# Optimization experiments

Measured on AMD Instinct MI355X. Metric: run time of the kernel, lower is better.

Reference implementation:

```python
import jax, jax.numpy as jnp
import numpy as np

B, S, DIM = 4, 2048, 1024


def _xavier(key, shape):
    # xavier_uniform for a [out, in] Linear weight
    fan_in, fan_out = shape[1], shape[0]
    limit = float(np.sqrt(6.0 / (fan_in + fan_out)))
    return jax.random.uniform(key, shape, jnp.float32, -limit, limit)


def setup_inputs() -> dict:
    key = jax.random.key(0)
    ks = jax.random.split(key, 8)
    z_real = jax.random.normal(ks[0], (B, S, DIM), jnp.float32)
    z_imag = jax.random.normal(ks[1], (B, S, DIM), jnp.float32)
    wq_r = _xavier(ks[2], (DIM, DIM))
    wq_i = _xavier(ks[3], (DIM, DIM))
    wk_r = _xavier(ks[4], (DIM, DIM))
    wk_i = _xavier(ks[5], (DIM, DIM))
    wv_r = _xavier(ks[6], (DIM, DIM))
    wv_i = _xavier(ks[7], (DIM, DIM))
    # causal mask (0 = masked), broadcast over batch
    mask = jnp.tril(jnp.ones((S, S), jnp.int32))
    return {"z_real": z_real, "z_imag": z_imag,
            "wq_r": wq_r, "wq_i": wq_i,
            "wk_r": wk_r, "wk_i": wk_i,
            "wv_r": wv_r, "wv_i": wv_i,
            "mask": mask}


def _complex_linear(xr, xi, wr, wi):
    # torch Linear: y = x @ W^T
    yr = xr @ wr.T - xi @ wi.T
    yi = xi @ wr.T + xr @ wi.T
    return yr, yi


def reference(z_real, z_imag, wq_r, wq_i, wk_r, wk_i, wv_r, wv_i, mask):
    dim = z_real.shape[-1]
    scale = dim ** (-0.5)
    qr, qi = _complex_linear(z_real, z_imag, wq_r, wq_i)
    kr, ki = _complex_linear(z_real, z_imag, wk_r, wk_i)
    vr, vi = _complex_linear(z_real, z_imag, wv_r, wv_i)
    # cat([q.real, q.imag]) @ cat([k.real, k.imag])^T == qr@kr^T + qi@ki^T
    scores = (jnp.einsum('bsd,btd->bst', qr, kr)
              + jnp.einsum('bsd,btd->bst', qi, ki)) * scale  # [B,S,S]
    scores = jnp.where(mask == 0, -jnp.inf, scores)
    attn = jax.nn.softmax(scores, axis=-1)
    out_r = jnp.einsum('bst,btd->bsd', attn, vr)
    out_i = jnp.einsum('bst,btd->bsd', attn, vi)
    return jnp.stack([out_r, out_i], axis=0)  # [2,B,S,dim] = (real, imag)
```

## Files before the change

kernel.cpp:

```cpp
#include <hip/hip_runtime.h>
#include <hip/hip_bf16.h>
#include <hip/hip_fp16.h>

#define DIMK 1024
#define SEQ  2048
#define BATCH 4
#define NTOK (BATCH*SEQ)
#define PROJ_ELEMS ((size_t)NTOK*DIMK)
#define LD 2048

typedef unsigned short ushort_t;
typedef __attribute__((ext_vector_type(8))) short short8;
typedef __attribute__((ext_vector_type(4))) float float4v;

__device__ __forceinline__ unsigned short f2bf(float f) {
    union { float f; unsigned int i; } x; x.f = f;
    unsigned int r = x.i + 0x7fffu + ((x.i >> 16) & 1u);
    return (unsigned short)(r >> 16);
}

__device__ __forceinline__ void gld_lds16(const void* g, void* l) {
    auto gp = reinterpret_cast<const __attribute__((address_space(1))) unsigned int*>(
        reinterpret_cast<uintptr_t>(g));
    auto lp = reinterpret_cast<__attribute__((address_space(3))) unsigned int*>(
        reinterpret_cast<uintptr_t>(l));
    __builtin_amdgcn_global_load_lds(gp, lp, 16, 0, 0);
}

__device__ __forceinline__ void gemm_core(
    const ushort_t* __restrict__ Arow,
    const ushort_t* __restrict__ Brow,
    int kbeg, int kend,
    ushort_t* Asm, ushort_t* Bsm,
    float4v acc[4][4], int wave, int lane)
{
    const int g  = lane >> 2;
    const int sx = lane & 3;
    const int scol = (((sx - (g >> 1)) & 3)) * 8;
    const int sc0 = wave * 2, sc1 = wave * 2 + 1;
    const int r16  = lane & 15;
    const int quad = lane >> 4;
    const int swz  = ((quad + (r16 >> 1)) & 3) * 8;
    const int cA = (wave >> 1) * 4;
    const int cB = (wave & 1) * 4;

    for (int k0 = kbeg; k0 < kend; k0 += 64) {
        #pragma unroll
        for (int h = 0; h < 2; ++h) {
            const int kh = k0 + h * 32;
            ushort_t* Ah = Asm + h * 4096;
            ushort_t* Bh = Bsm + h * 4096;
            gld_lds16(Arow + (size_t)(sc0 * 16 + g) * LD + kh + scol, Ah + sc0 * 512);
            gld_lds16(Arow + (size_t)(sc1 * 16 + g) * LD + kh + scol, Ah + sc1 * 512);
            gld_lds16(Brow + (size_t)(sc0 * 16 + g) * LD + kh + scol, Bh + sc0 * 512);
            gld_lds16(Brow + (size_t)(sc1 * 16 + g) * LD + kh + scol, Bh + sc1 * 512);
        }
        __syncthreads();
        #pragma unroll
        for (int h = 0; h < 2; ++h) {
            const ushort_t* Ah = Asm + h * 4096;
            const ushort_t* Bh = Bsm + h * 4096;
            short8 af[4], bfr[4];
            #pragma unroll
            for (int i = 0; i < 4; ++i)
                af[i] = *(const short8*)(Ah + (cA + i) * 512 + r16 * 32 + swz);
            #pragma unroll
            for (int j = 0; j < 4; ++j)
                bfr[j] = *(const short8*)(Bh + (cB + j) * 512 + r16 * 32 + swz);
            #pragma unroll
            for (int i = 0; i < 4; ++i)
                #pragma unroll
                for (int j = 0; j < 4; ++j)
                    acc[i][j] = __builtin_amdgcn_mfma_f32_16x16x32_bf16(af[i], bfr[j], acc[i][j], 0, 0, 0);
        }
        __syncthreads();
    }
}

__global__ __launch_bounds__(256, 2)
void gemm_proj(const ushort_t* __restrict__ A, const ushort_t* __restrict__ B,
               ushort_t* __restrict__ Cq, ushort_t* __restrict__ Ck,
               ushort_t* __restrict__ Cv)
{
    __shared__ ushort_t Asm[128 * 64], Bsm[128 * 64];
    const int tid = threadIdx.x, wave = tid >> 6, lane = tid & 63;
    const int m0 = blockIdx.y * 128;
    const int n0g = blockIdx.x * 128;
    ushort_t* C = (n0g < 2048) ? Cq : ((n0g < 4096) ? Ck : Cv);
    const int n0 = n0g & 2047;
    float4v acc[4][4] = {};
    gemm_core(A + (size_t)m0 * LD, B + (size_t)n0g * LD, 0, 2048, Asm, Bsm, acc, wave, lane);

    const int wm = (wave >> 1) * 64, wn = (wave & 1) * 64;
    const int col16 = lane & 15, quad = lane >> 4;
    #pragma unroll
    for (int i = 0; i < 4; ++i)
        #pragma unroll
        for (int j = 0; j < 4; ++j) {
            const int n = n0 + wn + j * 16 + col16;
            #pragma unroll
            for (int r = 0; r < 4; ++r) {
                const int m = m0 + wm + i * 16 + quad * 4 + r;
                C[(size_t)m * LD + n] = f2bf(acc[i][j][r]);
            }
        }
}

__global__ __launch_bounds__(256, 2)
void gemm_scores(const ushort_t* __restrict__ Q, const ushort_t* __restrict__ K,
                 __half* __restrict__ S)
{
    const int jt = blockIdx.x, it = blockIdx.y, b = blockIdx.z;
    if (jt > it) return;
    __shared__ ushort_t Asm[128 * 64], Bsm[128 * 64];
    const int tid = threadIdx.x, wave = tid >> 6, lane = tid & 63;
    const size_t boff = (size_t)b * SEQ * LD;
    float4v acc[4][4] = {};
    gemm_core(Q + boff + (size_t)it * 128 * LD, K + boff + (size_t)jt * 128 * LD,
              0, 2048, Asm, Bsm, acc, wave, lane);

    const int wm = (wave >> 1) * 64, wn = (wave & 1) * 64;
    const int col16 = lane & 15, quad = lane >> 4;
    const float scale = 0.03125f;
    __half* Sb = S + (size_t)b * SEQ * SEQ;
    #pragma unroll
    for (int i = 0; i < 4; ++i)
        #pragma unroll
        for (int j = 0; j < 4; ++j) {
            const int t = jt * 128 + wn + j * 16 + col16;
            #pragma unroll
            for (int r = 0; r < 4; ++r) {
                const int s = it * 128 + wm + i * 16 + quad * 4 + r;
                Sb[(size_t)s * SEQ + t] = __float2half(acc[i][j][r] * scale);
            }
        }
}

__global__ __launch_bounds__(256, 2)
void gemm_pv(const ushort_t* __restrict__ P, const ushort_t* __restrict__ VT,
             float* __restrict__ out)
{
    const int nt = blockIdx.x, mt = blockIdx.y, b = blockIdx.z;
    __shared__ ushort_t Asm[128 * 64], Bsm[128 * 64];
    const int tid = threadIdx.x, wave = tid >> 6, lane = tid & 63;
    const int kend = (mt + 1) * 128;
    float4v acc[4][4] = {};
    gemm_core(P + (size_t)b * SEQ * SEQ + (size_t)mt * 128 * LD,
              VT + (size_t)b * LD * LD + (size_t)nt * 128 * LD,
              0, kend, Asm, Bsm, acc, wave, lane);

    const int wm = (wave >> 1) * 64, wn = (wave & 1) * 64;
    const int col16 = lane & 15, quad = lane >> 4;
    #pragma unroll
    for (int i = 0; i < 4; ++i)
        #pragma unroll
        for (int j = 0; j < 4; ++j) {
            const int n = nt * 128 + wn + j * 16 + col16;
            float* dst = out + ((n < 1024) ? 0 : PROJ_ELEMS);
            const int d = n & 1023;
            #pragma unroll
            for (int r = 0; r < 4; ++r) {
                const int s = mt * 128 + wm + i * 16 + quad * 4 + r;
                dst[((size_t)b * SEQ + s) * DIMK + d] = acc[i][j][r];
            }
        }
}

__global__ __launch_bounds__(256)
void zcat_kernel(const float* __restrict__ zr, const float* __restrict__ zi,
                 ushort_t* __restrict__ zcat)
{
    const size_t e = ((size_t)blockIdx.x * 256 + threadIdx.x) * 8;
    const size_t tok = e >> 11;
    const int c = (int)(e & 2047);
    const float* src = (c < 1024) ? (zr + tok * 1024 + c) : (zi + tok * 1024 + (c - 1024));
    float4 a = *(const float4*)src;
    float4 b = *(const float4*)(src + 4);
    ushort_t* d = zcat + e;
    d[0]=f2bf(a.x); d[1]=f2bf(a.y); d[2]=f2bf(a.z); d[3]=f2bf(a.w);
    d[4]=f2bf(b.x); d[5]=f2bf(b.y); d[6]=f2bf(b.z); d[7]=f2bf(b.w);
}

__global__ __launch_bounds__(256)
void wstack_kernel(const float* __restrict__ wr, const float* __restrict__ wi,
                   ushort_t* __restrict__ ws)
{
    const size_t e = ((size_t)blockIdx.x * 256 + threadIdx.x) * 8;
    const int n = (int)(e >> 11), c = (int)(e & 2047);
    const int n1 = n & 1023, c1 = c & 1023;
    const float* src;
    float sgn = 1.f;
    if (n < 1024) {
        if (c < 1024) src = wr + (size_t)n1 * 1024 + c1;
        else        { src = wi + (size_t)n1 * 1024 + c1; sgn = -1.f; }
    } else {
        src = ((c < 1024) ? wi : wr) + (size_t)n1 * 1024 + c1;
    }
    float4 a = *(const float4*)src;
    float4 b = *(const float4*)(src + 4);
    ushort_t* d = ws + e;
    d[0]=f2bf(sgn*a.x); d[1]=f2bf(sgn*a.y); d[2]=f2bf(sgn*a.z); d[3]=f2bf(sgn*a.w);
    d[4]=f2bf(sgn*b.x); d[5]=f2bf(sgn*b.y); d[6]=f2bf(sgn*b.z); d[7]=f2bf(sgn*b.w);
}

__global__ __launch_bounds__(256)
void transpose_v(const ushort_t* __restrict__ vcat, ushort_t* __restrict__ vt)
{
    __shared__ ushort_t tile[64][65];
    const int b = blockIdx.z;
    const int t0 = blockIdx.x * 64, c0 = blockIdx.y * 64;
    const int tid = threadIdx.x;
    const int r = tid >> 4, c4 = (tid & 15) * 4;
    const ushort_t* src = vcat + ((size_t)(b * SEQ + t0)) * LD + c0;
    #pragma unroll
    for (int p = 0; p < 4; ++p) {
        const int row = p * 16 + r;
        ushort4 v = *(const ushort4*)(src + (size_t)row * LD + c4);
        tile[row][c4+0]=v.x; tile[row][c4+1]=v.y; tile[row][c4+2]=v.z; tile[row][c4+3]=v.w;
    }
    __syncthreads();
    ushort_t* dst = vt + ((size_t)b * LD + c0) * LD + t0;
    #pragma unroll
    for (int p = 0; p < 4; ++p) {
        const int crow = p * 16 + r;
        ushort4 v;
        v.x = tile[c4+0][crow]; v.y = tile[c4+1][crow];
        v.z = tile[c4+2][crow]; v.w = tile[c4+3][crow];
        *(ushort4*)(dst + (size_t)crow * LD + c4) = v;
    }
}

__global__ __launch_bounds__(256)
void softmax_kernel(__half* __restrict__ sc)
{
    const int row = blockIdx.x;
    const int s = row & (SEQ - 1);
    __half* x = sc + (size_t)row * SEQ;
    ushort_t* xo = (ushort_t*)x;
    const int n = s + 1;
    const int tid = threadIdx.x, wave = tid >> 6, lane = tid & 63;
    __shared__ float redm[4], reds[4];

    float m = -1e30f;
    for (int i = tid; i < n; i += 256) m = fmaxf(m, __half2float(x[i]));
    #pragma unroll
    for (int off = 32; off > 0; off >>= 1) m = fmaxf(m, __shfl_down(m, off, 64));
    if (lane == 0) redm[wave] = m;
    __syncthreads();
    if (tid == 0) redm[0] = fmaxf(fmaxf(redm[0], redm[1]), fmaxf(redm[2], redm[3]));
    __syncthreads();
    m = redm[0];

    float l = 0.f;
    for (int i = tid; i < n; i += 256) l += __expf(__half2float(x[i]) - m);
    #pragma unroll
    for (int off = 32; off > 0; off >>= 1) l += __shfl_down(l, off, 64);
    if (lane == 0) reds[wave] = l;
    __syncthreads();
    if (tid == 0) reds[0] = reds[0] + reds[1] + reds[2] + reds[3];
    __syncthreads();
    const float inv = 1.0f / reds[0];

    const int npad = min(SEQ, ((s >> 7) + 1) << 7);
    for (int i = tid; i < npad; i += 256) {
        float v = (i < n) ? __expf(__half2float(x[i]) - m) * inv : 0.f;
        xo[i] = f2bf(v);
    }
}

extern "C" void kernel_launch(void* const* d_in, const int* in_sizes, int n_in,
                              void* d_out, int out_size, void* d_ws, size_t ws_size,
                              hipStream_t stream)
{
    const float* z_real = (const float*)d_in[0];
    const float* z_imag = (const float*)d_in[1];
    const float* wq_r   = (const float*)d_in[2];
    const float* wq_i   = (const float*)d_in[3];
    const float* wk_r   = (const float*)d_in[4];
    const float* wk_i   = (const float*)d_in[5];
    const float* wv_r   = (const float*)d_in[6];
    const float* wv_i   = (const float*)d_in[7];

    uint8_t* ws = (uint8_t*)d_ws;
    ushort_t* zcat = (ushort_t*)(ws + 0);
    ushort_t* wall = (ushort_t*)(ws + 33554432);
    ushort_t* wsq  = wall;
    ushort_t* wsk  = (ushort_t*)(ws + 33554432 + 8388608);
    ushort_t* wsv  = (ushort_t*)(ws + 33554432 + 16777216);
    ushort_t* qcat = (ushort_t*)(ws + 58720256);
    ushort_t* kcat = (ushort_t*)(ws + 92274688);
    ushort_t* vcat = (ushort_t*)(ws + 125829120);
    ushort_t* vt   = (ushort_t*)(ws + 0);
    __half*   sc   = (__half*)(ws + 125829120);
    float*    outp = (float*)d_out;

    zcat_kernel<<<dim3(8192), dim3(256), 0, stream>>>(z_real, z_imag, zcat);
    wstack_kernel<<<dim3(2048), dim3(256), 0, stream>>>(wq_r, wq_i, wsq);
    wstack_kernel<<<dim3(2048), dim3(256), 0, stream>>>(wk_r, wk_i, wsk);
    wstack_kernel<<<dim3(2048), dim3(256), 0, stream>>>(wv_r, wv_i, wsv);

    gemm_proj<<<dim3(48, 64), dim3(256), 0, stream>>>(zcat, wall, qcat, kcat, vcat);

    transpose_v<<<dim3(32, 32, 4), dim3(256), 0, stream>>>(vcat, vt);
    gemm_scores<<<dim3(16, 16, 4), dim3(256), 0, stream>>>(qcat, kcat, sc);
    softmax_kernel<<<dim3(NTOK), dim3(256), 0, stream>>>(sc);
    gemm_pv<<<dim3(16, 16, 4), dim3(256), 0, stream>>>((ushort_t*)sc, vt, outp);
}
```

Measured before the change: 550.5 us.

## Use 256x256 tiles with 8 waves and double-buffered LDS pipelining in GEMMs

Replaces the 128x128, 4-wave GEMM core with a 256x256, 8-wave core. The new core double-buffers LDS with async global-to-LDS loads, so the next K-slab is prefetched while MFMAs run, and it interleaves fine-grained barriers with s_setprio to raise MFMA priority. The larger tiles raise arithmetic intensity and cut global traffic. The cost is 128KB of LDS per block, larger accumulators that may pressure registers, and coarser causal granularity that wastes more work on masked blocks. The softmax zero-padding is widened to 256 to match the new tile size.

```diff
diff --git a/kernel.cpp b/kernel.cpp
--- a/kernel.cpp
+++ b/kernel.cpp
@@ -13,6 +13,8 @@
 typedef __attribute__((ext_vector_type(8))) short short8;
 typedef __attribute__((ext_vector_type(4))) float float4v;
 
+#define MFMA_BF16 __builtin_amdgcn_mfma_f32_16x16x32_bf16
+
 __device__ __forceinline__ unsigned short f2bf(float f) {
     union { float f; unsigned int i; } x; x.f = f;
     unsigned int r = x.i + 0x7fffu + ((x.i >> 16) & 1u);
@@ -27,140 +29,216 @@
     __builtin_amdgcn_global_load_lds(gp, lp, 16, 0, 0);
 }
 
-__device__ __forceinline__ void gemm_core(
+__device__ __forceinline__ void stage2(const ushort_t* __restrict__ gbase,
+                                       ushort_t* lbase, int kcol,
+                                       int rg0, int g, int scol)
+{
+    gld_lds16(gbase + (size_t)(rg0 * 16 + g) * LD + kcol + scol,
+              lbase + rg0 * 512);
+    gld_lds16(gbase + (size_t)(rg0 * 16 + 16 + g) * LD + kcol + scol,
+              lbase + rg0 * 512 + 512);
+}
+
+__device__ __forceinline__ void gemm_core256(
     const ushort_t* __restrict__ Arow,
     const ushort_t* __restrict__ Brow,
-    int kbeg, int kend,
-    ushort_t* Asm, ushort_t* Bsm,
-    float4v acc[4][4], int wave, int lane)
-{
-    const int g  = lane >> 2;
-    const int sx = lane & 3;
-    const int scol = (((sx - (g >> 1)) & 3)) * 8;
-    const int sc0 = wave * 2, sc1 = wave * 2 + 1;
+    int kend,
+    ushort_t* Alds, ushort_t* Blds,
+    float4v acc[8][4], int wid, int lane)
+{
+    const int g    = lane >> 2;
+    const int sx   = lane & 3;
+    const int scol = ((sx - (g >> 1)) & 3) * 8;
     const int r16  = lane & 15;
     const int quad = lane >> 4;
-    const int swz  = ((quad + (r16 >> 1)) & 3) * 8;
-    const int cA = (wave >> 1) * 4;
-    const int cB = (wave & 1) * 4;
-
-    for (int k0 = kbeg; k0 < kend; k0 += 64) {
-        #pragma unroll
-        for (int h = 0; h < 2; ++h) {
-            const int kh = k0 + h * 32;
-            ushort_t* Ah = Asm + h * 4096;
-            ushort_t* Bh = Bsm + h * 4096;
-            gld_lds16(Arow + (size_t)(sc0 * 16 + g) * LD + kh + scol, Ah + sc0 * 512);
-            gld_lds16(Arow + (size_t)(sc1 * 16 + g) * LD + kh + scol, Ah + sc1 * 512);
-            gld_lds16(Brow + (size_t)(sc0 * 16 + g) * LD + kh + scol, Bh + sc0 * 512);
-            gld_lds16(Brow + (size_t)(sc1 * 16 + g) * LD + kh + scol, Bh + sc1 * 512);
-        }
-        __syncthreads();
-        #pragma unroll
-        for (int h = 0; h < 2; ++h) {
-            const ushort_t* Ah = Asm + h * 4096;
-            const ushort_t* Bh = Bsm + h * 4096;
-            short8 af[4], bfr[4];
-            #pragma unroll
-            for (int i = 0; i < 4; ++i)
-                af[i] = *(const short8*)(Ah + (cA + i) * 512 + r16 * 32 + swz);
+    const int roff = r16 * 32 + ((quad + (r16 >> 1)) & 3) * 8;
+    const int wm = wid >> 2, wn = wid & 3;
+    const int rg0 = wid * 2;
+    const int NT = kend >> 6;
+
+    stage2(Brow, Blds,        0,  rg0, g, scol);
+    stage2(Arow, Alds,        0,  rg0, g, scol);
+    stage2(Brow, Blds + 8192, 32, rg0, g, scol);
+    stage2(Arow, Alds + 8192, 32, rg0, g, scol);
+    asm volatile("s_waitcnt vmcnt(4)" ::: "memory");
+    __builtin_amdgcn_s_barrier();
+
+    for (int t = 0; t < NT; ++t) {
+        const int d     = (t & 1) << 14;
+        const int dn    = d ^ 16384;
+        const int knext = (t + 1) << 6;
+        const bool pre  = (t + 1 < NT);
+        short8 af[4], bf[4];
+
+        #pragma unroll
+        for (int j = 0; j < 4; ++j)
+            bf[j] = *(const short8*)(Blds + d + (wn * 4 + j) * 512 + roff);
+        #pragma unroll
+        for (int ii = 0; ii < 4; ++ii)
+            af[ii] = *(const short8*)(Alds + d + (wm * 8 + ii) * 512 + roff);
+        if (pre) stage2(Brow, Blds + dn, knext, rg0, g, scol);
+        asm volatile("" ::: "memory");
+        __builtin_amdgcn_s_barrier();
+        asm volatile("s_waitcnt lgkmcnt(0)" ::: "memory");
+        __builtin_amdgcn_s_setprio(1);
+        #pragma unroll
+        for (int ii = 0; ii < 4; ++ii)
             #pragma unroll
             for (int j = 0; j < 4; ++j)
-                bfr[j] = *(const short8*)(Bh + (cB + j) * 512 + r16 * 32 + swz);
-            #pragma unroll
-            for (int i = 0; i < 4; ++i)
-                #pragma unroll
-                for (int j = 0; j < 4; ++j)
-                    acc[i][j] = __builtin_amdgcn_mfma_f32_16x16x32_bf16(af[i], bfr[j], acc[i][j], 0, 0, 0);
-        }
-        __syncthreads();
-    }
-}
-
-__global__ __launch_bounds__(256, 2)
+                acc[ii][j] = MFMA_BF16(af[ii], bf[j], acc[ii][j], 0, 0, 0);
+        __builtin_amdgcn_s_setprio(0);
+        asm volatile("" ::: "memory");
+        __builtin_amdgcn_s_barrier();
+
+        #pragma unroll
+        for (int ii = 0; ii < 4; ++ii)
+            af[ii] = *(const short8*)(Alds + d + (wm * 8 + 4 + ii) * 512 + roff);
+        if (pre) {
+            stage2(Arow, Alds + dn, knext, rg0, g, scol);
+            asm volatile("s_waitcnt vmcnt(4)" ::: "memory");
+        } else {
+            asm volatile("s_waitcnt vmcnt(0)" ::: "memory");
+        }
+        __builtin_amdgcn_s_barrier();
+        asm volatile("s_waitcnt lgkmcnt(0)" ::: "memory");
+        __builtin_amdgcn_s_setprio(1);
+        #pragma unroll
+        for (int ii = 0; ii < 4; ++ii)
+            #pragma unroll
+            for (int j = 0; j < 4; ++j)
+                acc[4 + ii][j] = MFMA_BF16(af[ii], bf[j], acc[4 + ii][j], 0, 0, 0);
+        __builtin_amdgcn_s_setprio(0);
+        asm volatile("" ::: "memory");
+        __builtin_amdgcn_s_barrier();
+
+        #pragma unroll
+        for (int j = 0; j < 4; ++j)
+            bf[j] = *(const short8*)(Blds + d + 8192 + (wn * 4 + j) * 512 + roff);
+        #pragma unroll
+        for (int ii = 0; ii < 4; ++ii)
+            af[ii] = *(const short8*)(Alds + d + 8192 + (wm * 8 + ii) * 512 + roff);
+        if (pre) stage2(Brow, Blds + dn + 8192, knext + 32, rg0, g, scol);
+        asm volatile("" ::: "memory");
+        __builtin_amdgcn_s_barrier();
+        asm volatile("s_waitcnt lgkmcnt(0)" ::: "memory");
+        __builtin_amdgcn_s_setprio(1);
+        #pragma unroll
+        for (int ii = 0; ii < 4; ++ii)
+            #pragma unroll
+            for (int j = 0; j < 4; ++j)
+                acc[ii][j] = MFMA_BF16(af[ii], bf[j], acc[ii][j], 0, 0, 0);
+        __builtin_amdgcn_s_setprio(0);
+        asm volatile("" ::: "memory");
+        __builtin_amdgcn_s_barrier();
+
+        #pragma unroll
+        for (int ii = 0; ii < 4; ++ii)
+            af[ii] = *(const short8*)(Alds + d + 8192 + (wm * 8 + 4 + ii) * 512 + roff);
+        if (pre) {
+            stage2(Arow, Alds + dn + 8192, knext + 32, rg0, g, scol);
+            asm volatile("s_waitcnt vmcnt(4)" ::: "memory");
+        } else {
+            asm volatile("" ::: "memory");
+        }
+        __builtin_amdgcn_s_barrier();
+        asm volatile("s_waitcnt lgkmcnt(0)" ::: "memory");
+        __builtin_amdgcn_s_setprio(1);
+        #pragma unroll
+        for (int ii = 0; ii < 4; ++ii)
+            #pragma unroll
+            for (int j = 0; j < 4; ++j)
+                acc[4 + ii][j] = MFMA_BF16(af[ii], bf[j], acc[4 + ii][j], 0, 0, 0);
+        __builtin_amdgcn_s_setprio(0);
+        asm volatile("" ::: "memory");
+        __builtin_amdgcn_s_barrier();
+    }
+}
+
+__global__ __launch_bounds__(512, 2)
 void gemm_proj(const ushort_t* __restrict__ A, const ushort_t* __restrict__ B,
                ushort_t* __restrict__ Cq, ushort_t* __restrict__ Ck,
                ushort_t* __restrict__ Cv)
 {
-    __shared__ ushort_t Asm[128 * 64], Bsm[128 * 64];
-    const int tid = threadIdx.x, wave = tid >> 6, lane = tid & 63;
-    const int m0 = blockIdx.y * 128;
-    const int n0g = blockIdx.x * 128;
+    __shared__ ushort_t smem[65536];
+    const int tid = threadIdx.x, wid = tid >> 6, lane = tid & 63;
+    const int m0 = blockIdx.y * 256;
+    const int n0g = blockIdx.x * 256;
     ushort_t* C = (n0g < 2048) ? Cq : ((n0g < 4096) ? Ck : Cv);
     const int n0 = n0g & 2047;
-    float4v acc[4][4] = {};
-    gemm_core(A + (size_t)m0 * LD, B + (size_t)n0g * LD, 0, 2048, Asm, Bsm, acc, wave, lane);
-
-    const int wm = (wave >> 1) * 64, wn = (wave & 1) * 64;
+    float4v acc[8][4] = {};
+    gemm_core256(A + (size_t)m0 * LD, B + (size_t)n0g * LD, 2048,
+                 smem, smem + 32768, acc, wid, lane);
+
+    const int wm = wid >> 2, wn = wid & 3;
     const int col16 = lane & 15, quad = lane >> 4;
     #pragma unroll
-    for (int i = 0; i < 4; ++i)
+    for (int i = 0; i < 8; ++i)
         #pragma unroll
         for (int j = 0; j < 4; ++j) {
-            const int n = n0 + wn + j * 16 + col16;
+            const int n = n0 + wn * 64 + j * 16 + col16;
             #pragma unroll
             for (int r = 0; r < 4; ++r) {
-                const int m = m0 + wm + i * 16 + quad * 4 + r;
+                const int m = m0 + wm * 128 + i * 16 + quad * 4 + r;
                 C[(size_t)m * LD + n] = f2bf(acc[i][j][r]);
             }
         }
 }
 
-__global__ __launch_bounds__(256, 2)
+__global__ __launch_bounds__(512, 2)
 void gemm_scores(const ushort_t* __restrict__ Q, const ushort_t* __restrict__ K,
                  __half* __restrict__ S)
 {
     const int jt = blockIdx.x, it = blockIdx.y, b = blockIdx.z;
     if (jt > it) return;
-    __shared__ ushort_t Asm[128 * 64], Bsm[128 * 64];
-    const int tid = threadIdx.x, wave = tid >> 6, lane = tid & 63;
+    __shared__ ushort_t smem[65536];
+    const int tid = threadIdx.x, wid = tid >> 6, lane = tid & 63;
     const size_t boff = (size_t)b * SEQ * LD;
-    float4v acc[4][4] = {};
-    gemm_core(Q + boff + (size_t)it * 128 * LD, K + boff + (size_t)jt * 128 * LD,
-              0, 2048, Asm, Bsm, acc, wave, lane);
-
-    const int wm = (wave >> 1) * 64, wn = (wave & 1) * 64;
+    float4v acc[8][4] = {};
+    gemm_core256(Q + boff + (size_t)it * 256 * LD, K + boff + (size_t)jt * 256 * LD,
+                 2048, smem, smem + 32768, acc, wid, lane);
+
+    const int wm = wid >> 2, wn = wid & 3;
     const int col16 = lane & 15, quad = lane >> 4;
     const float scale = 0.03125f;
     __half* Sb = S + (size_t)b * SEQ * SEQ;
     #pragma unroll
-    for (int i = 0; i < 4; ++i)
+    for (int i = 0; i < 8; ++i)
         #pragma unroll
         for (int j = 0; j < 4; ++j) {
-            const int t = jt * 128 + wn + j * 16 + col16;
+            const int t = jt * 256 + wn * 64 + j * 16 + col16;
             #pragma unroll
             for (int r = 0; r < 4; ++r) {
-                const int s = it * 128 + wm + i * 16 + quad * 4 + r;
+                const int s = it * 256 + wm * 128 + i * 16 + quad * 4 + r;
                 Sb[(size_t)s * SEQ + t] = __float2half(acc[i][j][r] * scale);
             }
         }
 }
 
-__global__ __launch_bounds__(256, 2)
+__global__ __launch_bounds__(512, 2)
 void gemm_pv(const ushort_t* __restrict__ P, const ushort_t* __restrict__ VT,
              float* __restrict__ out)
 {
     const int nt = blockIdx.x, mt = blockIdx.y, b = blockIdx.z;
-    __shared__ ushort_t Asm[128 * 64], Bsm[128 * 64];
-    const int tid = threadIdx.x, wave = tid >> 6, lane = tid & 63;
-    const int kend = (mt + 1) * 128;
-    float4v acc[4][4] = {};
-    gemm_core(P + (size_t)b * SEQ * SEQ + (size_t)mt * 128 * LD,
-              VT + (size_t)b * LD * LD + (size_t)nt * 128 * LD,
-              0, kend, Asm, Bsm, acc, wave, lane);
-
-    const int wm = (wave >> 1) * 64, wn = (wave & 1) * 64;
+    __shared__ ushort_t smem[65536];
+    const int tid = threadIdx.x, wid = tid >> 6, lane = tid & 63;
+    const int kend = (mt + 1) * 256;
+    float4v acc[8][4] = {};
+    gemm_core256(P + (size_t)b * SEQ * SEQ + (size_t)mt * 256 * LD,
+                 VT + (size_t)b * LD * LD + (size_t)nt * 256 * LD,
+                 kend, smem, smem + 32768, acc, wid, lane);
+
+    const int wm = wid >> 2, wn = wid & 3;
     const int col16 = lane & 15, quad = lane >> 4;
     #pragma unroll
-    for (int i = 0; i < 4; ++i)
+    for (int i = 0; i < 8; ++i)
         #pragma unroll
         for (int j = 0; j < 4; ++j) {
-            const int n = nt * 128 + wn + j * 16 + col16;
+            const int n = nt * 256 + wn * 64 + j * 16 + col16;
             float* dst = out + ((n < 1024) ? 0 : PROJ_ELEMS);
             const int d = n & 1023;
             #pragma unroll
             for (int r = 0; r < 4; ++r) {
-                const int s = mt * 128 + wm + i * 16 + quad * 4 + r;
+                const int s = mt * 256 + wm * 128 + i * 16 + quad * 4 + r;
                 dst[((size_t)b * SEQ + s) * DIMK + d] = acc[i][j][r];
             }
         }
@@ -261,7 +339,7 @@
     __syncthreads();
     const float inv = 1.0f / reds[0];
 
-    const int npad = min(SEQ, ((s >> 7) + 1) << 7);
+    const int npad = min(SEQ, ((s >> 8) + 1) << 8);
     for (int i = tid; i < npad; i += 256) {
         float v = (i < n) ? __expf(__half2float(x[i]) - m) * inv : 0.f;
         xo[i] = f2bf(v);
@@ -299,10 +377,10 @@
     wstack_kernel<<<dim3(2048), dim3(256), 0, stream>>>(wk_r, wk_i, wsk);
     wstack_kernel<<<dim3(2048), dim3(256), 0, stream>>>(wv_r, wv_i, wsv);
 
-    gemm_proj<<<dim3(48, 64), dim3(256), 0, stream>>>(zcat, wall, qcat, kcat, vcat);
+    gemm_proj<<<dim3(24, 32), dim3(512), 0, stream>>>(zcat, wall, qcat, kcat, vcat);
 
     transpose_v<<<dim3(32, 32, 4), dim3(256), 0, stream>>>(vcat, vt);
-    gemm_scores<<<dim3(16, 16, 4), dim3(256), 0, stream>>>(qcat, kcat, sc);
+    gemm_scores<<<dim3(8, 8, 4), dim3(512), 0, stream>>>(qcat, kcat, sc);
     softmax_kernel<<<dim3(NTOK), dim3(256), 0, stream>>>(sc);
-    gemm_pv<<<dim3(16, 16, 4), dim3(256), 0, stream>>>((ushort_t*)sc, vt, outp);
-}
+    gemm_pv<<<dim3(8, 8, 4), dim3(512), 0, stream>>>((ushort_t*)sc, vt, outp);
+}
```

Measured after the change: 491.3 us. 1.12x faster.
